# Kernel tuning notes

Measured on AMD Instinct MI355X. Metric: run time of the kernel, lower is better.

The kernel has to match this reference:

```python
import jax, jax.numpy as jnp
import numpy as np

N, D_IN, D_OUT, B = 200000, 256, 256, 256

def setup_inputs() -> dict:
    key = jax.random.key(0)
    k1, k2, k3, k4, k5 = jax.random.split(key, 5)
    lim = float(np.sqrt(6.0 / (D_IN + D_OUT)))  # xavier_init scale=1
    return {
        "nodes": jax.random.normal(k1, (N, D_IN), dtype=jnp.float32),
        "owner_masks": jax.random.randint(k2, (B, N), 0, 2, dtype=jnp.int32),
        "Wt": jax.random.uniform(k3, (D_OUT, D_IN), jnp.float32, -lim, lim),
        "bt": jax.random.normal(k4, (D_OUT,), dtype=jnp.float32),
        "Wg": jax.random.uniform(k5, (D_OUT, D_IN), jnp.float32, -lim, lim),
        "bg": jnp.ones((D_OUT,), dtype=jnp.float32),  # gate bias init fill_(1)
    }

def reference(nodes, owner_masks, Wt, bt, Wg, bg):
    # gates = sigmoid(Linear(nodes)); data = Linear(nodes)  -> [N, D_OUT]
    gates = jax.nn.sigmoid(nodes @ Wg.T + bg)
    data = nodes @ Wt.T + bt
    # owner-mask matmul == masked scatter-sum over nodes -> [B, D_OUT]
    fmask = owner_masks.astype(jnp.float32)
    res = jnp.einsum('bn,nd->bd', fmask, data * gates)
    return res  # dropout is identity in eval mode
```

## Files before the change

### kernel.cpp

```cpp
#include <hip/hip_runtime.h>
#include <stdint.h>

#define NND 200000

typedef unsigned short u16;
typedef __attribute__((ext_vector_type(4))) float f4;
typedef __attribute__((ext_vector_type(4))) int   i4;
typedef __attribute__((ext_vector_type(8))) short s8;
typedef __attribute__((ext_vector_type(4))) short s4;
typedef __attribute__((ext_vector_type(4))) float acc4;

__device__ __forceinline__ short f2bf(float f) {
    union { float f; uint32_t u; } v; v.f = f;
    uint32_t r = v.u + 0x7FFFu + ((v.u >> 16) & 1u);
    return (short)(r >> 16);
}

__device__ __forceinline__ void gld16(const void* g, const void* l) {
    __builtin_amdgcn_global_load_lds(
        (const __attribute__((address_space(1))) void*)g,
        (__attribute__((address_space(3))) void*)l, 16, 0, 0);
}

__global__ __launch_bounds__(256) void k_prep(const float* __restrict__ Wt,
                                              const float* __restrict__ Wg,
                                              u16* __restrict__ wtb,
                                              u16* __restrict__ wgb) {
    int i = blockIdx.x * 256 + threadIdx.x;
    wtb[i] = (u16)f2bf(Wt[i]);
    wgb[i] = (u16)f2bf(Wg[i]);
}

__global__ __launch_bounds__(256) void k_h(const float* __restrict__ nodes,
                                           const u16* __restrict__ wtb,
                                           const u16* __restrict__ wgb,
                                           const float* __restrict__ btp,
                                           const float* __restrict__ bgp,
                                           u16* __restrict__ h_t) {
    __shared__ __align__(16) float As[128 * 64];
    __shared__ __align__(16) u16 Bs[2][64 * 64];

    const int tid  = threadIdx.x;
    const int lane = tid & 63, wave = tid >> 6;
    const int quad = lane >> 4, l16 = lane & 15;
    const int d0 = blockIdx.x * 64;
    const int n0 = blockIdx.y * 128;
    const int wm = wave & 1;
    const int wd = wave >> 1;

    acc4 at_[4][2], ag_[4][2];
#pragma unroll
    for (int rt = 0; rt < 4; ++rt)
#pragma unroll
        for (int dt = 0; dt < 2; ++dt) { at_[rt][dt] = (acc4)0.0f; ag_[rt][dt] = (acc4)0.0f; }

    for (int kt = 0; kt < 4; ++kt) {
        const int k0 = kt * 64;
#pragma unroll
        for (int i = 0; i < 8; ++i) {
            int g = i * 256 + tid;
            int row = g >> 4, c = g & 15;
            int srow = n0 + row; srow = srow < NND ? srow : (NND - 1);
            gld16(nodes + (size_t)srow * 256 + k0 + ((c ^ (row & 15)) << 2), As + g * 4);
        }
#pragma unroll
        for (int i = 0; i < 2; ++i) {
            int g = i * 256 + tid;
            int dr = g >> 3, c = g & 7;
            size_t off = (size_t)(d0 + dr) * 256 + k0 + ((c ^ (dr & 7)) << 3);
            gld16(wtb + off, &Bs[0][g * 8]);
            gld16(wgb + off, &Bs[1][g * 8]);
        }
        __syncthreads();
#pragma unroll
        for (int ks = 0; ks < 2; ++ks) {
            s8 af[4];
#pragma unroll
            for (int rt = 0; rt < 4; ++rt) {
                int row = wm * 64 + rt * 16 + l16;
                int gi = ks * 8 + quad * 2;
                const float* base = As + row * 64;
                f4 a0 = *(const f4*)(base + ((gi ^ l16) << 2));
                f4 a1 = *(const f4*)(base + (((gi + 1) ^ l16) << 2));
                s8 t;
                t[0] = f2bf(a0.x); t[1] = f2bf(a0.y); t[2] = f2bf(a0.z); t[3] = f2bf(a0.w);
                t[4] = f2bf(a1.x); t[5] = f2bf(a1.y); t[6] = f2bf(a1.z); t[7] = f2bf(a1.w);
                af[rt] = t;
            }
#pragma unroll
            for (int dt = 0; dt < 2; ++dt) {
                int d = wd * 32 + dt * 16 + l16;
                int slot = (ks * 4 + quad) ^ (l16 & 7);
                s8 bT = *(const s8*)&Bs[0][d * 64 + slot * 8];
                s8 bG = *(const s8*)&Bs[1][d * 64 + slot * 8];
#pragma unroll
                for (int rt = 0; rt < 4; ++rt) {
                    at_[rt][dt] = __builtin_amdgcn_mfma_f32_16x16x32_bf16(af[rt], bT, at_[rt][dt], 0, 0, 0);
                    ag_[rt][dt] = __builtin_amdgcn_mfma_f32_16x16x32_bf16(af[rt], bG, ag_[rt][dt], 0, 0, 0);
                }
            }
        }
        __syncthreads();
    }

    u16* Hs = (u16*)As;
#pragma unroll
    for (int dt = 0; dt < 2; ++dt) {
        int dl = wd * 32 + dt * 16 + l16;
        float btv = btp[d0 + dl], bgv = bgp[d0 + dl];
#pragma unroll
        for (int rt = 0; rt < 4; ++rt) {
            s4 hv;
#pragma unroll
            for (int r = 0; r < 4; ++r) {
                float dat = at_[rt][dt][r] + btv;
                float gat = ag_[rt][dt][r] + bgv;
                float sg = 1.0f / (1.0f + __expf(-gat));
                hv[r] = f2bf(dat * sg);
            }
            *(s4*)&Hs[dl * 136 + wm * 64 + rt * 16 + quad * 4] = hv;
        }
    }
    __syncthreads();
#pragma unroll
    for (int i = 0; i < 4; ++i) {
        int g = i * 256 + tid;
        int dl = g >> 4, c = g & 15;
        int n = n0 + c * 8;
        if (n < NND) {
            f4 v = *(const f4*)&Hs[dl * 136 + c * 8];
            *(f4*)(h_t + (size_t)(d0 + dl) * NND + n) = v;
        }
    }
}

__global__ __launch_bounds__(256) void k_res(const int* __restrict__ masks,
                                             const u16* __restrict__ h_t,
                                             float* __restrict__ outp) {
    __shared__ __align__(16) int Ms[128 * 64];
    __shared__ __align__(16) u16 Hs[128 * 64];

    const int tid  = threadIdx.x;
    const int lane = tid & 63, wave = tid >> 6;
    const int quad = lane >> 4, l16 = lane & 15;
    const int b0 = (blockIdx.x & 1) * 128;
    const int d0 = (blockIdx.x >> 1) * 128;
    const int wm = wave & 1, wd = wave >> 1;

    acc4 acc[4][4];
#pragma unroll
    for (int rt = 0; rt < 4; ++rt)
#pragma unroll
        for (int dt = 0; dt < 4; ++dt) acc[rt][dt] = (acc4)0.0f;

    for (int it = 0; it < 25; ++it) {
        const int nb = blockIdx.y * 1600 + it * 64;
#pragma unroll
        for (int i = 0; i < 8; ++i) {
            int g = i * 256 + tid;
            int row = g >> 4, c = g & 15;
            gld16(masks + (size_t)(b0 + row) * NND + nb + ((c ^ (row & 15)) << 2), Ms + g * 4);
        }
#pragma unroll
        for (int i = 0; i < 4; ++i) {
            int g = i * 256 + tid;
            int dr = g >> 3, c = g & 7;
            gld16(h_t + (size_t)(d0 + dr) * NND + nb + ((c ^ (dr & 7)) << 3), Hs + g * 8);
        }
        __syncthreads();
#pragma unroll
        for (int ks = 0; ks < 2; ++ks) {
            s8 af[4];
#pragma unroll
            for (int rt = 0; rt < 4; ++rt) {
                int row = wm * 64 + rt * 16 + l16;
                int gi = ks * 8 + quad * 2;
                const int* base = Ms + row * 64;
                i4 m0 = *(const i4*)(base + ((gi ^ l16) << 2));
                i4 m1 = *(const i4*)(base + (((gi + 1) ^ l16) << 2));
                s8 t;
                t[0] = (short)((-m0.x) & 0x3F80); t[1] = (short)((-m0.y) & 0x3F80);
                t[2] = (short)((-m0.z) & 0x3F80); t[3] = (short)((-m0.w) & 0x3F80);
                t[4] = (short)((-m1.x) & 0x3F80); t[5] = (short)((-m1.y) & 0x3F80);
                t[6] = (short)((-m1.z) & 0x3F80); t[7] = (short)((-m1.w) & 0x3F80);
                af[rt] = t;
            }
#pragma unroll
            for (int dt = 0; dt < 4; ++dt) {
                int d = wd * 64 + dt * 16 + l16;
                int slot = (ks * 4 + quad) ^ (l16 & 7);
                s8 bf_ = *(const s8*)&Hs[d * 64 + slot * 8];
#pragma unroll
                for (int rt = 0; rt < 4; ++rt)
                    acc[rt][dt] = __builtin_amdgcn_mfma_f32_16x16x32_bf16(af[rt], bf_, acc[rt][dt], 0, 0, 0);
            }
        }
        __syncthreads();
    }
#pragma unroll
    for (int rt = 0; rt < 4; ++rt)
#pragma unroll
        for (int dt = 0; dt < 4; ++dt) {
            int d  = d0 + wd * 64 + dt * 16 + l16;
            int bb = b0 + wm * 64 + rt * 16 + quad * 4;
#pragma unroll
            for (int r = 0; r < 4; ++r)
                atomicAdd(outp + (size_t)(bb + r) * 256 + d, acc[rt][dt][r]);
        }
}

extern "C" void kernel_launch(void* const* d_in, const int* in_sizes, int n_in,
                              void* d_out, int out_size, void* d_ws, size_t ws_size,
                              hipStream_t stream) {
    const float* nodes = (const float*)d_in[0];
    const int*   masks = (const int*)d_in[1];
    const float* Wt    = (const float*)d_in[2];
    const float* bt    = (const float*)d_in[3];
    const float* Wg    = (const float*)d_in[4];
    const float* bg    = (const float*)d_in[5];
    float* outp = (float*)d_out;

    u16* h_t = (u16*)d_ws;
    u16* wtb = (u16*)((char*)d_ws + (size_t)102400000);
    u16* wgb = wtb + 65536;

    hipMemsetAsync(d_out, 0, (size_t)out_size * sizeof(float), stream);
    k_prep<<<dim3(256), dim3(256), 0, stream>>>(Wt, Wg, wtb, wgb);
    k_h<<<dim3(4, 1563), dim3(256), 0, stream>>>(nodes, wtb, wgb, bt, bg, h_t);
    k_res<<<dim3(4, 125), dim3(256), 0, stream>>>(masks, h_t, outp);
}
```

Measured before the change: 565.0 us.

## Retile both GEMM kernels so each block covers all output columns

k_h now gives each block 64 nodes and all 256 output features. Node rows are read only once, converted to bf16 in registers and stored packed in LDS, where before they were reread by four column blocks and converted on every LDS read. k_res now has each block cover all 256 features, so the masks are read once rather than twice, and it packs masks to bf16 before the LDS store. In exchange it uses larger accumulator tiles and more LDS, which raises register pressure (launch_bounds 256,2) and may lower occupancy.

```diff
diff --git a/kernel.cpp b/kernel.cpp
--- a/kernel.cpp
+++ b/kernel.cpp
@@ -6,8 +6,8 @@
 typedef unsigned short u16;
 typedef __attribute__((ext_vector_type(4))) float f4;
 typedef __attribute__((ext_vector_type(4))) int   i4;
+typedef __attribute__((ext_vector_type(2))) unsigned int u2;
 typedef __attribute__((ext_vector_type(8))) short s8;
-typedef __attribute__((ext_vector_type(4))) short s4;
 typedef __attribute__((ext_vector_type(4))) float acc4;
 
 __device__ __forceinline__ short f2bf(float f) {
@@ -15,8 +15,13 @@
     uint32_t r = v.u + 0x7FFFu + ((v.u >> 16) & 1u);
     return (short)(r >> 16);
 }
-
-__device__ __forceinline__ void gld16(const void* g, const void* l) {
+__device__ __forceinline__ uint32_t pack2bf(float a, float b) {
+    uint32_t ua = __float_as_uint(a), ub = __float_as_uint(b);
+    ua = ua + 0x7FFFu + ((ua >> 16) & 1u);
+    ub = ub + 0x7FFFu + ((ub >> 16) & 1u);
+    return (ua >> 16) | (ub & 0xFFFF0000u);
+}
+__device__ __forceinline__ void gld16(const void* g, void* l) {
     __builtin_amdgcn_global_load_lds(
         (const __attribute__((address_space(1))) void*)g,
         (__attribute__((address_space(3))) void*)l, 16, 0, 0);
@@ -31,68 +36,65 @@
     wgb[i] = (u16)f2bf(Wg[i]);
 }
 
-__global__ __launch_bounds__(256) void k_h(const float* __restrict__ nodes,
-                                           const u16* __restrict__ wtb,
-                                           const u16* __restrict__ wgb,
-                                           const float* __restrict__ btp,
-                                           const float* __restrict__ bgp,
-                                           u16* __restrict__ h_t) {
-    __shared__ __align__(16) float As[128 * 64];
-    __shared__ __align__(16) u16 Bs[2][64 * 64];
+__global__ __launch_bounds__(256, 2) void k_h(const float* __restrict__ nodes,
+                                              const u16* __restrict__ wtb,
+                                              const u16* __restrict__ wgb,
+                                              const float* __restrict__ btp,
+                                              const float* __restrict__ bgp,
+                                              u16* __restrict__ h_t) {
+    __shared__ __align__(16) char smem[74752];
+    u16* Abf = (u16*)smem;
+    u16* Ws0 = (u16*)(smem + 9216);
+    u16* Ws1 = (u16*)(smem + 41984);
 
     const int tid  = threadIdx.x;
     const int lane = tid & 63, wave = tid >> 6;
     const int quad = lane >> 4, l16 = lane & 15;
-    const int d0 = blockIdx.x * 64;
-    const int n0 = blockIdx.y * 128;
-    const int wm = wave & 1;
-    const int wd = wave >> 1;
-
-    acc4 at_[4][2], ag_[4][2];
+    const int n0 = blockIdx.x * 64;
+
+    acc4 at_[4][4], ag_[4][4];
 #pragma unroll
     for (int rt = 0; rt < 4; ++rt)
 #pragma unroll
-        for (int dt = 0; dt < 2; ++dt) { at_[rt][dt] = (acc4)0.0f; ag_[rt][dt] = (acc4)0.0f; }
+        for (int dt = 0; dt < 4; ++dt) { at_[rt][dt] = (acc4)0.0f; ag_[rt][dt] = (acc4)0.0f; }
 
     for (int kt = 0; kt < 4; ++kt) {
         const int k0 = kt * 64;
+        f4 av[4];
+#pragma unroll
+        for (int i = 0; i < 4; ++i) {
+            int f = i * 256 + tid;
+            int row = f >> 4, kp = f & 15;
+            av[i] = *(const f4*)(nodes + (size_t)(n0 + row) * 256 + k0 + kp * 4);
+        }
 #pragma unroll
         for (int i = 0; i < 8; ++i) {
             int g = i * 256 + tid;
-            int row = g >> 4, c = g & 15;
-            int srow = n0 + row; srow = srow < NND ? srow : (NND - 1);
-            gld16(nodes + (size_t)srow * 256 + k0 + ((c ^ (row & 15)) << 2), As + g * 4);
-        }
-#pragma unroll
-        for (int i = 0; i < 2; ++i) {
-            int g = i * 256 + tid;
             int dr = g >> 3, c = g & 7;
-            size_t off = (size_t)(d0 + dr) * 256 + k0 + ((c ^ (dr & 7)) << 3);
-            gld16(wtb + off, &Bs[0][g * 8]);
-            gld16(wgb + off, &Bs[1][g * 8]);
+            size_t off = (size_t)dr * 256 + k0 + ((c ^ (dr & 7)) << 3);
+            gld16(wtb + off, Ws0 + g * 8);
+            gld16(wgb + off, Ws1 + g * 8);
+        }
+#pragma unroll
+        for (int i = 0; i < 4; ++i) {
+            int f = i * 256 + tid;
+            int row = f >> 4, kp = f & 15;
+            u2 p; p.x = pack2bf(av[i].x, av[i].y); p.y = pack2bf(av[i].z, av[i].w);
+            *(u2*)((char*)Abf + row * 144 + kp * 8) = p;
         }
         __syncthreads();
 #pragma unroll
         for (int ks = 0; ks < 2; ++ks) {
             s8 af[4];
 #pragma unroll
-            for (int rt = 0; rt < 4; ++rt) {
-                int row = wm * 64 + rt * 16 + l16;
-                int gi = ks * 8 + quad * 2;
-                const float* base = As + row * 64;
-                f4 a0 = *(const f4*)(base + ((gi ^ l16) << 2));
-                f4 a1 = *(const f4*)(base + (((gi + 1) ^ l16) << 2));
-                s8 t;
-                t[0] = f2bf(a0.x); t[1] = f2bf(a0.y); t[2] = f2bf(a0.z); t[3] = f2bf(a0.w);
-                t[4] = f2bf(a1.x); t[5] = f2bf(a1.y); t[6] = f2bf(a1.z); t[7] = f2bf(a1.w);
-                af[rt] = t;
-            }
-#pragma unroll
-            for (int dt = 0; dt < 2; ++dt) {
-                int d = wd * 32 + dt * 16 + l16;
-                int slot = (ks * 4 + quad) ^ (l16 & 7);
-                s8 bT = *(const s8*)&Bs[0][d * 64 + slot * 8];
-                s8 bG = *(const s8*)&Bs[1][d * 64 + slot * 8];
+            for (int rt = 0; rt < 4; ++rt)
+                af[rt] = *(const s8*)((char*)Abf + (rt * 16 + l16) * 144 + ks * 64 + quad * 16);
+#pragma unroll
+            for (int dt = 0; dt < 4; ++dt) {
+                int dl = wave * 64 + dt * 16 + l16;
+                int slot = (ks * 4 + quad) ^ (dl & 7);
+                s8 bT = *(const s8*)(Ws0 + dl * 64 + slot * 8);
+                s8 bG = *(const s8*)(Ws1 + dl * 64 + slot * 8);
 #pragma unroll
                 for (int rt = 0; rt < 4; ++rt) {
                     at_[rt][dt] = __builtin_amdgcn_mfma_f32_16x16x32_bf16(af[rt], bT, at_[rt][dt], 0, 0, 0);
@@ -103,69 +105,72 @@
         __syncthreads();
     }
 
-    u16* Hs = (u16*)As;
-#pragma unroll
-    for (int dt = 0; dt < 2; ++dt) {
-        int dl = wd * 32 + dt * 16 + l16;
-        float btv = btp[d0 + dl], bgv = bgp[d0 + dl];
+    u16* Hs = (u16*)smem;
+#pragma unroll
+    for (int dt = 0; dt < 4; ++dt) {
+        int dl = wave * 64 + dt * 16 + l16;
+        float btv = btp[dl], bgv = bgp[dl];
 #pragma unroll
         for (int rt = 0; rt < 4; ++rt) {
-            s4 hv;
-#pragma unroll
-            for (int r = 0; r < 4; ++r) {
-                float dat = at_[rt][dt][r] + btv;
-                float gat = ag_[rt][dt][r] + bgv;
-                float sg = 1.0f / (1.0f + __expf(-gat));
-                hv[r] = f2bf(dat * sg);
-            }
-            *(s4*)&Hs[dl * 136 + wm * 64 + rt * 16 + quad * 4] = hv;
+            float h0, h1, h2, h3;
+            float g0 = ag_[rt][dt][0] + bgv, g1 = ag_[rt][dt][1] + bgv;
+            float g2 = ag_[rt][dt][2] + bgv, g3 = ag_[rt][dt][3] + bgv;
+            h0 = (at_[rt][dt][0] + btv) / (1.0f + __expf(-g0));
+            h1 = (at_[rt][dt][1] + btv) / (1.0f + __expf(-g1));
+            h2 = (at_[rt][dt][2] + btv) / (1.0f + __expf(-g2));
+            h3 = (at_[rt][dt][3] + btv) / (1.0f + __expf(-g3));
+            u2 p; p.x = pack2bf(h0, h1); p.y = pack2bf(h2, h3);
+            *(u2*)((char*)Hs + dl * 144 + (rt * 16 + quad * 4) * 2) = p;
         }
     }
     __syncthreads();
 #pragma unroll
-    for (int i = 0; i < 4; ++i) {
+    for (int i = 0; i < 8; ++i) {
         int g = i * 256 + tid;
-        int dl = g >> 4, c = g & 15;
-        int n = n0 + c * 8;
-        if (n < NND) {
-            f4 v = *(const f4*)&Hs[dl * 136 + c * 8];
-            *(f4*)(h_t + (size_t)(d0 + dl) * NND + n) = v;
-        }
-    }
-}
-
-__global__ __launch_bounds__(256) void k_res(const int* __restrict__ masks,
-                                             const u16* __restrict__ h_t,
-                                             float* __restrict__ outp) {
-    __shared__ __align__(16) int Ms[128 * 64];
-    __shared__ __align__(16) u16 Hs[128 * 64];
+        int d = g >> 3, c = g & 7;
+        f4 v = *(const f4*)((char*)Hs + d * 144 + c * 16);
+        *(f4*)(h_t + (size_t)d * NND + n0 + c * 8) = v;
+    }
+}
+
+__global__ __launch_bounds__(256, 2) void k_res(const int* __restrict__ masks,
+                                                const u16* __restrict__ h_t,
+                                                float* __restrict__ outp) {
+    __shared__ __align__(16) u16 Ms[128 * 64];
+    __shared__ __align__(16) u16 Hs[256 * 64];
 
     const int tid  = threadIdx.x;
     const int lane = tid & 63, wave = tid >> 6;
     const int quad = lane >> 4, l16 = lane & 15;
-    const int b0 = (blockIdx.x & 1) * 128;
-    const int d0 = (blockIdx.x >> 1) * 128;
-    const int wm = wave & 1, wd = wave >> 1;
-
-    acc4 acc[4][4];
+    const int b0 = blockIdx.x * 128;
+    const int wb = wave & 1, wd = wave >> 1;
+
+    acc4 acc[4][8];
 #pragma unroll
     for (int rt = 0; rt < 4; ++rt)
 #pragma unroll
-        for (int dt = 0; dt < 4; ++dt) acc[rt][dt] = (acc4)0.0f;
+        for (int dt = 0; dt < 8; ++dt) acc[rt][dt] = (acc4)0.0f;
 
     for (int it = 0; it < 25; ++it) {
         const int nb = blockIdx.y * 1600 + it * 64;
 #pragma unroll
         for (int i = 0; i < 8; ++i) {
             int g = i * 256 + tid;
-            int row = g >> 4, c = g & 15;
-            gld16(masks + (size_t)(b0 + row) * NND + nb + ((c ^ (row & 15)) << 2), Ms + g * 4);
+            int dr = g >> 3, c = g & 7;
+            gld16(h_t + (size_t)dr * NND + nb + ((c ^ (dr & 7)) << 3), (char*)Hs + g * 16);
         }
 #pragma unroll
         for (int i = 0; i < 4; ++i) {
             int g = i * 256 + tid;
             int dr = g >> 3, c = g & 7;
-            gld16(h_t + (size_t)(d0 + dr) * NND + nb + ((c ^ (dr & 7)) << 3), Hs + g * 8);
+            const i4* mp = (const i4*)(masks + (size_t)(b0 + dr) * NND + nb + c * 8);
+            i4 m0 = mp[0], m1 = mp[1];
+            i4 w;
+            w.x = (int)((((uint32_t)(-m0.x)) & 0x3F80u) | ((((uint32_t)(-m0.y)) & 0x3F80u) << 16));
+            w.y = (int)((((uint32_t)(-m0.z)) & 0x3F80u) | ((((uint32_t)(-m0.w)) & 0x3F80u) << 16));
+            w.z = (int)((((uint32_t)(-m1.x)) & 0x3F80u) | ((((uint32_t)(-m1.y)) & 0x3F80u) << 16));
+            w.w = (int)((((uint32_t)(-m1.z)) & 0x3F80u) | ((((uint32_t)(-m1.w)) & 0x3F80u) << 16));
+            *(i4*)((char*)Ms + dr * 128 + ((c ^ (dr & 7)) << 4)) = w;
         }
         __syncthreads();
 #pragma unroll
@@ -173,23 +178,13 @@
             s8 af[4];
 #pragma unroll
             for (int rt = 0; rt < 4; ++rt) {
-                int row = wm * 64 + rt * 16 + l16;
-                int gi = ks * 8 + quad * 2;
-                const int* base = Ms + row * 64;
-                i4 m0 = *(const i4*)(base + ((gi ^ l16) << 2));
-                i4 m1 = *(const i4*)(base + (((gi + 1) ^ l16) << 2));
-                s8 t;
-                t[0] = (short)((-m0.x) & 0x3F80); t[1] = (short)((-m0.y) & 0x3F80);
-                t[2] = (short)((-m0.z) & 0x3F80); t[3] = (short)((-m0.w) & 0x3F80);
-                t[4] = (short)((-m1.x) & 0x3F80); t[5] = (short)((-m1.y) & 0x3F80);
-                t[6] = (short)((-m1.z) & 0x3F80); t[7] = (short)((-m1.w) & 0x3F80);
-                af[rt] = t;
+                int r = wb * 64 + rt * 16 + l16;
+                af[rt] = *(const s8*)((char*)Ms + r * 128 + (((ks * 4 + quad) ^ (r & 7)) << 4));
             }
 #pragma unroll
-            for (int dt = 0; dt < 4; ++dt) {
-                int d = wd * 64 + dt * 16 + l16;
-                int slot = (ks * 4 + quad) ^ (l16 & 7);
-                s8 bf_ = *(const s8*)&Hs[d * 64 + slot * 8];
+            for (int dt = 0; dt < 8; ++dt) {
+                int dl = wd * 128 + dt * 16 + l16;
+                s8 bf_ = *(const s8*)((char*)Hs + dl * 128 + (((ks * 4 + quad) ^ (dl & 7)) << 4));
 #pragma unroll
                 for (int rt = 0; rt < 4; ++rt)
                     acc[rt][dt] = __builtin_amdgcn_mfma_f32_16x16x32_bf16(af[rt], bf_, acc[rt][dt], 0, 0, 0);
@@ -200,12 +195,12 @@
 #pragma unroll
     for (int rt = 0; rt < 4; ++rt)
 #pragma unroll
-        for (int dt = 0; dt < 4; ++dt) {
-            int d  = d0 + wd * 64 + dt * 16 + l16;
-            int bb = b0 + wm * 64 + rt * 16 + quad * 4;
+        for (int dt = 0; dt < 8; ++dt) {
+            int b = b0 + wb * 64 + rt * 16 + quad * 4;
+            int d = wd * 128 + dt * 16 + l16;
 #pragma unroll
             for (int r = 0; r < 4; ++r)
-                atomicAdd(outp + (size_t)(bb + r) * 256 + d, acc[rt][dt][r]);
+                atomicAdd(outp + (size_t)(b + r) * 256 + d, acc[rt][dt][r]);
         }
 }
 
@@ -226,6 +221,6 @@
 
     hipMemsetAsync(d_out, 0, (size_t)out_size * sizeof(float), stream);
     k_prep<<<dim3(256), dim3(256), 0, stream>>>(Wt, Wg, wtb, wgb);
-    k_h<<<dim3(4, 1563), dim3(256), 0, stream>>>(nodes, wtb, wgb, bt, bg, h_t);
-    k_res<<<dim3(4, 125), dim3(256), 0, stream>>>(masks, h_t, outp);
-}
+    k_h<<<dim3(3125), dim3(256), 0, stream>>>(nodes, wtb, wgb, bt, bg, h_t);
+    k_res<<<dim3(2, 125), dim3(256), 0, stream>>>(masks, h_t, outp);
+}
```

Result: faster. 523.9 us (-7.3%).
